# Performance work log

Hardware: AMD Instinct MI355X
Metric: run time of the kernel (lower is better)

The kernel has to match this reference:

```python
import jax, jax.numpy as jnp
import numpy as np

EMA_DECAY = 0.99
LOSS_SCALE = 10.0
COMMIT_COEF = 0.25
EPS = 1e-5


def setup_inputs() -> dict:
    key = jax.random.key(0)
    k1, k2, k3 = jax.random.split(key, 3)
    B, S, D, K = 8, 2048, 256, 4096
    z = jax.random.normal(k1, (B, S, D), dtype=jnp.float32)
    attention_mask = jnp.ones((B, S), dtype=jnp.float32)
    codebook = jax.random.normal(k2, (K, D), dtype=jnp.float32)
    ema_count = jnp.ones((K,), dtype=jnp.float32)
    ema_weight = codebook.copy()  # torch: ema_weight = codebook.weight.data.clone()
    return {"z": z, "attention_mask": attention_mask, "codebook": codebook,
            "ema_count": ema_count, "ema_weight": ema_weight}


def reference(z, attention_mask, codebook, ema_count, ema_weight):
    B, S, D = z.shape
    K = codebook.shape[0]
    flat = z.reshape(-1, D)                       # [N, D], N = B*S
    # squared euclidean distances to codebook: [N, K]
    distances = (jnp.sum(flat * flat, axis=1, keepdims=True)
                 - 2.0 * flat @ codebook.T
                 + jnp.sum(codebook * codebook, axis=1))
    indices = jnp.argmin(distances, axis=1)       # [N] int
    quantized = codebook[indices].reshape(B, S, D)

    # EMA accumulation (training path). Instead of materializing the NxK
    # one-hot and doing encodings.T @ flat, use segment sums (same math).
    mask_flat = attention_mask.reshape(-1)        # [N]
    n = jax.ops.segment_sum(mask_flat, indices, num_segments=K)            # [K]
    dw = jax.ops.segment_sum(flat * mask_flat[:, None], indices,
                             num_segments=K)                               # [K, D]

    new_count = ema_count * EMA_DECAY + (1.0 - EMA_DECAY) * n
    total = jnp.sum(new_count)
    new_count = (new_count + EPS) / (total + K * EPS) * total
    new_weight = ema_weight * EMA_DECAY + (1.0 - EMA_DECAY) * dw

    # commitment loss (quantized detached)
    loss_tok = jnp.mean((z - jax.lax.stop_gradient(quantized)) ** 2, axis=-1)  # [B,S]
    quantize_loss = LOSS_SCALE * COMMIT_COEF * jnp.sum(loss_tok * attention_mask) / jnp.sum(attention_mask)

    # straight-through estimator
    out = z + jax.lax.stop_gradient(quantized - z)
    return out, indices, quantize_loss, new_count, new_weight
```

## Files before the change

### kernel.cpp

```cpp
#include <hip/hip_runtime.h>
#include <hip/hip_fp16.h>
#include <cstdint>
#include <cstddef>


#define N_TOK 16384
#define DIM   256
#define K_CB  4096

typedef _Float16 h8    __attribute__((ext_vector_type(8)));
typedef float    f32x4 __attribute__((ext_vector_type(4)));
typedef float    f32x16 __attribute__((ext_vector_type(16)));

#define WS_ZF      0u
#define WS_CP      8388608u
#define WS_CN      10485760u
#define WS_NRM     10502144u
#define WS_CAND    10630144u
#define WS_IDX     12727296u
#define WS_COUNT   12792832u
#define WS_START   12809216u
#define WS_CURSOR  12825616u
#define WS_SORTED  12842000u
#define WS_NACC    16921600u
#define WS_NB      16937984u
#define WS_LPART   16938000u
#define WS_MPART   16954384u
#define WS_NBPART  16970768u

__device__ __forceinline__ void gload_lds16(const void* g, void* l) {
  __builtin_amdgcn_global_load_lds(
      (const __attribute__((address_space(1))) uint32_t*)g,
      (__attribute__((address_space(3))) uint32_t*)l, 16, 0, 0);
}

__global__ void vq_split_z(const float* __restrict__ z, unsigned short* __restrict__ zf,
                           float2* __restrict__ nrm) {
  int t = blockIdx.x * 256 + threadIdx.x;
  int tok = t >> 5, c = t & 31;
  const float4* zp = reinterpret_cast<const float4*>(z) + (size_t)tok * 64 + c * 2;
  float4 va = zp[0], vb = zp[1];
  float x[8] = {va.x, va.y, va.z, va.w, vb.x, vb.y, vb.z, vb.w};
  union { _Float16 h[8]; uint4 u; } a;
  float s1 = 0.f, s2 = 0.f;
#pragma unroll
  for (int i = 0; i < 8; ++i) {
    _Float16 h1 = (_Float16)x[i];
    float lo = (x[i] - (float)h1) * 2048.0f;
    a.h[i] = h1;
    s1 += (float)h1 * (float)h1;
    s2 += lo * lo;
  }
  size_t off = (size_t)(tok >> 7) * 65536u + (size_t)(c >> 1) * 4096u
             + (size_t)(tok & 127) * 32u + (size_t)(c & 1) * 16u;
  *reinterpret_cast<uint4*>((unsigned char*)zf + off) = a.u;
#pragma unroll
  for (int o = 1; o < 32; o <<= 1) { s1 += __shfl_xor(s1, o); s2 += __shfl_xor(s2, o); }
  if (c == 0) nrm[tok] = make_float2(sqrtf(s1), sqrtf(s2));
}

__global__ void vq_split_c(const float* __restrict__ cb, unsigned short* __restrict__ cp1,
                           float* __restrict__ cn1, float2* __restrict__ nbpart) {
  __shared__ float sm1[4], sm2[4];
  int w = threadIdx.x >> 6, l = threadIdx.x & 63;
  int row = blockIdx.x * 4 + w;
  float4 v = reinterpret_cast<const float4*>(cb)[row * 64 + l];
  float x[4] = {v.x, v.y, v.z, v.w};
  union { _Float16 h[4]; ushort4 u; } a;
  double ss = 0.0;
  float s1 = 0.f, s2 = 0.f;
#pragma unroll
  for (int i = 0; i < 4; ++i) {
    _Float16 h1 = (_Float16)x[i];
    float lo = (x[i] - (float)h1) * 2048.0f;
    a.h[i] = h1;
    s1 += (float)h1 * (float)h1;
    s2 += lo * lo;
    ss += (double)x[i] * (double)x[i];
  }
  reinterpret_cast<ushort4*>(cp1)[row * 64 + l] = a.u;
  for (int off = 1; off < 64; off <<= 1) {
    s1 += __shfl_xor(s1, off); s2 += __shfl_xor(s2, off); ss += __shfl_xor(ss, off);
  }
  if (l == 0) {
    cn1[row] = (float)ss;
    sm1[w] = s1; sm2[w] = s2;
  }
  __syncthreads();
  if (threadIdx.x == 0) {
    float m1 = fmaxf(fmaxf(sm1[0], sm1[1]), fmaxf(sm1[2], sm1[3]));
    float m2 = fmaxf(fmaxf(sm2[0], sm2[1]), fmaxf(sm2[2], sm2[3]));
    nbpart[blockIdx.x] = make_float2(sqrtf(m1), sqrtf(m2));
  }
}

__global__ void vq_nb_reduce(const float2* __restrict__ nbpart, float* __restrict__ nb) {
  __shared__ float r1[256], r2[256];
  int tid = threadIdx.x;
  float m1 = 0.f, m2 = 0.f;
  for (int i = tid; i < 1024; i += 256) {
    float2 p = nbpart[i];
    m1 = fmaxf(m1, p.x); m2 = fmaxf(m2, p.y);
  }
  r1[tid] = m1; r2[tid] = m2; __syncthreads();
  for (int s = 128; s > 0; s >>= 1) {
    if (tid < s) { r1[tid] = fmaxf(r1[tid], r1[tid + s]); r2[tid] = fmaxf(r2[tid], r2[tid + s]); }
    __syncthreads();
  }
  if (tid == 0) { nb[0] = r1[0]; nb[1] = r2[0]; }
}

__global__ __launch_bounds__(256, 2) void vq_scan(
    const unsigned short* __restrict__ zf, const unsigned short* __restrict__ cp,
    const float* __restrict__ cn1, float4* __restrict__ cand) {
  __shared__ __align__(1024) unsigned char cbl[2][16384];
  __shared__ __align__(16) float cnl[2][32];

  const int bid  = blockIdx.x;
  const int wgid = (bid & 7) * 128 + (bid >> 3);
  const int tg   = wgid >> 3;
  const int es   = wgid & 7;
  const int tok0 = tg * 128;
  const int e0b  = es * 512;

  const int tx = threadIdx.x;
  const int w = tx >> 6, l = tx & 63;
  const int r = l & 31, h = l >> 5;

  const unsigned char* zg = (const unsigned char*)zf + (size_t)tg * 65536u
                            + (unsigned)(w * 1024 + r * 32 + h * 16);
  h8 zfr[16];
#pragma unroll
  for (int kt = 0; kt < 16; ++kt) {
    const void* p = zg + kt * 4096;
    asm volatile("global_load_dwordx4 %0, %1, off"
                 : "=v"(zfr[kt]) : "v"(p));
  }

  const unsigned char* cpb = (const unsigned char*)cp;

  float v1 = 3e38f, v2 = 3e38f;
  int   i1 = 0x7fffffff, i2 = 0x7fffffff;

#pragma unroll
  for (int j = 0; j < 4; ++j) {
    int row = (w * 4 + j) * 2 + h;
    int lc  = r ^ row;
    gload_lds16(cpb + (size_t)(e0b + row) * 512 + lc * 16,
                &cbl[0][(w * 4 + j) * 1024]);
  }
  if (tx < 8)
    gload_lds16((const unsigned char*)cn1 + (size_t)e0b * 4 + tx * 16, &cnl[0][0]);
  __syncthreads();

  for (int t = 0; t < 16; ++t) {
    const int b = t & 1;
    if (t < 15) {
      const int e0n = e0b + (t + 1) * 32;
#pragma unroll
      for (int j = 0; j < 4; ++j) {
        int row = (w * 4 + j) * 2 + h;
        int lc  = r ^ row;
        gload_lds16(cpb + (size_t)(e0n + row) * 512 + lc * 16,
                    &cbl[b ^ 1][(w * 4 + j) * 1024]);
      }
      if (tx < 8)
        gload_lds16((const unsigned char*)cn1 + (size_t)e0n * 4 + tx * 16,
                    &cnl[b ^ 1][0]);
    }

    f32x16 acc;
#pragma unroll
    for (int i = 0; i < 16; ++i) acc[i] = 0.f;
#pragma unroll
    for (int kt = 0; kt < 16; ++kt) {
      int sc = (kt * 2 + h) ^ r;
      h8 af = *reinterpret_cast<const h8*>(&cbl[b][r * 512 + sc * 16]);
      acc = __builtin_amdgcn_mfma_f32_32x32x16_f16(af, zfr[kt], acc, 0, 0, 0);
    }

    const int e0 = e0b + t * 32 + 4 * h;
#pragma unroll
    for (int g = 0; g < 4; ++g) {
      f32x4 cnv = *reinterpret_cast<const f32x4*>(&cnl[b][g * 8 + 4 * h]);
#pragma unroll
      for (int q = 0; q < 4; ++q) {
        float d = cnv[q] - 2.0f * acc[g * 4 + q];
        int   e = e0 + g * 8 + q;
        bool c1 = d < v1, c2 = d < v2;
        i2 = c1 ? i1 : (c2 ? e : i2);
        v2 = c1 ? v1 : (c2 ? d : v2);
        i1 = c1 ? e : i1;
        v1 = c1 ? d : v1;
      }
    }
    __syncthreads();
  }

  {
    float ov1 = __shfl_xor(v1, 32), ov2 = __shfl_xor(v2, 32);
    int   oi1 = __shfl_xor(i1, 32), oi2 = __shfl_xor(i2, 32);
    if (ov1 < v1 || (ov1 == v1 && oi1 < i1)) {
      v2 = v1; i2 = i1; v1 = ov1; i1 = oi1;
    } else if (ov1 < v2 || (ov1 == v2 && oi1 < i2)) {
      v2 = ov1; i2 = oi1;
    }
    if (ov2 < v1 || (ov2 == v1 && oi2 < i1)) {
      v2 = v1; i2 = i1; v1 = ov2; i1 = oi2;
    } else if (ov2 < v2 || (ov2 == v2 && oi2 < i2)) {
      v2 = ov2; i2 = oi2;
    }
    if (h == 0) {
      int token = tok0 + w * 32 + r;
      cand[(size_t)token * 8 + es] =
          make_float4(v1, v2, __int_as_float(i1), __int_as_float(i2));
    }
  }
}

__global__ void vq_merge(
    const float4* __restrict__ cand, const float* __restrict__ z,
    const float* __restrict__ mask, const float* __restrict__ codebook,
    const float2* __restrict__ nrm, const float* __restrict__ nb,
    float* __restrict__ out0, float* __restrict__ out_idx,
    int* __restrict__ idxs, int* __restrict__ count,
    float* __restrict__ loss_part, float* __restrict__ mask_part) {
  __shared__ float ls[4], ms[4];
  int w = threadIdx.x >> 6, l = threadIdx.x & 63;
  int token = blockIdx.x * 4 + w;

  float4 rec = cand[(size_t)token * 8 + (l & 7)];
  float rv1 = rec.x, rv2 = rec.y;
  int   ri1 = __float_as_int(rec.z), ri2 = __float_as_int(rec.w);
  float m_a = rv1;
  for (int o = 1; o < 8; o <<= 1) m_a = fminf(m_a, __shfl_xor(m_a, o));

  float2 nh = nrm[token];
  float NB1 = nb[0], NB2 = nb[1];
  float E = 2.0f * ((nh.x * NB2 + nh.y * NB1) * (1.0f / 2048.0f)
                    + nh.y * NB2 * (1.0f / 4194304.0f));
  float thr = m_a + 2.0f * E * 1.05f + 0.05f;

  float4 zv = reinterpret_cast<const float4*>(z)[(size_t)token * 64 + l];

  unsigned long long c1 = __ballot((l < 8) && (rv1 <= thr));
  unsigned long long c2 = __ballot((l < 8) && (rv2 <= thr));
  double bd = 1e300; int bi = 0x7fffffff;
  while (c1 | c2) {
    int k;
    if (c1) { int s = __ffsll(c1) - 1; c1 &= c1 - 1; k = __shfl(ri1, s); }
    else    { int s = __ffsll(c2) - 1; c2 &= c2 - 1; k = __shfl(ri2, s); }
    float4 cv = reinterpret_cast<const float4*>(codebook)[(size_t)k * 64 + l];
    double d0 = (double)zv.x - cv.x, d1 = (double)zv.y - cv.y;
    double d2 = (double)zv.z - cv.z, d3 = (double)zv.w - cv.w;
    double dd = d0 * d0 + d1 * d1 + d2 * d2 + d3 * d3;
    for (int o = 1; o < 64; o <<= 1) dd += __shfl_xor(dd, o);
    if (dd < bd || (dd == bd && k < bi)) { bd = dd; bi = k; }
  }

  float4 cv = reinterpret_cast<const float4*>(codebook)[(size_t)bi * 64 + l];
  reinterpret_cast<float4*>(out0)[(size_t)token * 64 + l] = cv;

  float mk = mask[token];
  if (l == 0) {
    out_idx[token] = (float)bi;
    idxs[token]    = bi;
    atomicAdd(&count[bi], 1);
    ls[w] = mk * (float)bd * (1.0f / 256.0f);
    ms[w] = mk;
  }
  __syncthreads();
  if (threadIdx.x == 0) {
    loss_part[blockIdx.x] = ls[0] + ls[1] + ls[2] + ls[3];
    mask_part[blockIdx.x] = ms[0] + ms[1] + ms[2] + ms[3];
  }
}

__global__ void vq_prescan(const int* __restrict__ count, int* __restrict__ start,
                           int* __restrict__ cursor) {
  __shared__ int wsum[256];
  int tid = threadIdx.x;
  int loc[16]; int s = 0;
#pragma unroll
  for (int i = 0; i < 16; ++i) { loc[i] = count[tid * 16 + i]; s += loc[i]; }
  wsum[tid] = s;
  __syncthreads();
  for (int off = 1; off < 256; off <<= 1) {
    int v = (tid >= off) ? wsum[tid - off] : 0;
    __syncthreads();
    wsum[tid] += v;
    __syncthreads();
  }
  int run = wsum[tid] - s;
#pragma unroll
  for (int i = 0; i < 16; ++i) {
    start[tid * 16 + i]  = run;
    cursor[tid * 16 + i] = run;
    run += loc[i];
  }
  if (tid == 255) start[K_CB] = wsum[255];
}

__global__ void vq_scatter(const int* __restrict__ idxs, int* __restrict__ cursor,
                           int* __restrict__ sorted) {
  int t = blockIdx.x * 256 + threadIdx.x;
  int k = idxs[t];
  int pos = atomicAdd(&cursor[k], 1);
  sorted[pos] = t;
}

__global__ __launch_bounds__(512) void vq_segsum(
    const int* __restrict__ start, const int* __restrict__ sorted,
    const float* __restrict__ z, const float* __restrict__ mask,
    const float* __restrict__ ew,
    float* __restrict__ out_weight, float* __restrict__ nacc) {
  __shared__ float4 red[8][64];
  __shared__ float nas[8];
  const int k = blockIdx.x;
  const int w = threadIdx.x >> 6, l = threadIdx.x & 63;
  const int s = start[k], e = start[k + 1];
  const float4* z4 = reinterpret_cast<const float4*>(z);

  float ax = 0.f, ay = 0.f, az = 0.f, aw = 0.f, na = 0.f;
  int i = s + w;
  for (; i + 8 < e; i += 16) {
    int t0 = sorted[i], t1 = sorted[i + 8];
    float mk0 = mask[t0], mk1 = mask[t1];
    float4 a4 = z4[(size_t)t0 * 64 + l];
    float4 b4 = z4[(size_t)t1 * 64 + l];
    ax += mk0 * a4.x + mk1 * b4.x;
    ay += mk0 * a4.y + mk1 * b4.y;
    az += mk0 * a4.z + mk1 * b4.z;
    aw += mk0 * a4.w + mk1 * b4.w;
    na += mk0 + mk1;
  }
  if (i < e) {
    int t0 = sorted[i];
    float mk0 = mask[t0];
    float4 a4 = z4[(size_t)t0 * 64 + l];
    ax += mk0 * a4.x; ay += mk0 * a4.y; az += mk0 * a4.z; aw += mk0 * a4.w;
    na += mk0;
  }
  red[w][l] = make_float4(ax, ay, az, aw);
  if (l == 0) nas[w] = na;
  __syncthreads();

  if (w == 0) {
    float4 a = red[0][l];
#pragma unroll
    for (int j = 1; j < 8; ++j) {
      float4 b = red[j][l];
      a.x += b.x; a.y += b.y; a.z += b.z; a.w += b.w;
    }
    float4 e4 = reinterpret_cast<const float4*>(ew)[(size_t)k * 64 + l];
    float4 o;
    o.x = 0.99f * e4.x + 0.01f * a.x;
    o.y = 0.99f * e4.y + 0.01f * a.y;
    o.z = 0.99f * e4.z + 0.01f * a.z;
    o.w = 0.99f * e4.w + 0.01f * a.w;
    reinterpret_cast<float4*>(out_weight)[(size_t)k * 64 + l] = o;
    if (l == 0) {
      float nn = 0.f;
#pragma unroll
      for (int j = 0; j < 8; ++j) nn += nas[j];
      nacc[k] = nn;
    }
  }
}

__global__ void vq_finish_count(const float* __restrict__ ec, const float* __restrict__ nacc,
                                const float* __restrict__ loss_part,
                                const float* __restrict__ mask_part,
                                float* __restrict__ out_count, float* __restrict__ out_loss) {
  __shared__ float nc_s[K_CB];
  __shared__ float red[256];
  int tid = threadIdx.x;
  float part = 0.f;
  for (int i = tid; i < K_CB; i += 256) {
    float nc = 0.99f * ec[i] + 0.01f * nacc[i];
    nc_s[i] = nc; part += nc;
  }
  red[tid] = part; __syncthreads();
  for (int s = 128; s > 0; s >>= 1) { if (tid < s) red[tid] += red[tid + s]; __syncthreads(); }
  float total = red[0];
  float scale = total / (total + (float)K_CB * 1e-5f);
  for (int i = tid; i < K_CB; i += 256) out_count[i] = (nc_s[i] + 1e-5f) * scale;
  __syncthreads();

  float ln = 0.f, lm = 0.f;
  for (int i = tid; i < 4096; i += 256) { ln += loss_part[i]; lm += mask_part[i]; }
  red[tid] = ln; __syncthreads();
  for (int s = 128; s > 0; s >>= 1) { if (tid < s) red[tid] += red[tid + s]; __syncthreads(); }
  ln = red[0]; __syncthreads();
  red[tid] = lm; __syncthreads();
  for (int s = 128; s > 0; s >>= 1) { if (tid < s) red[tid] += red[tid + s]; __syncthreads(); }
  lm = red[0];
  if (tid == 0) out_loss[0] = 2.5f * ln / lm;
}

extern "C" void kernel_launch(void* const* d_in, const int* in_sizes, int n_in,
                              void* d_out, int out_size, void* d_ws, size_t ws_size,
                              hipStream_t stream) {
  const float* z          = (const float*)d_in[0];
  const float* mask       = (const float*)d_in[1];
  const float* codebook   = (const float*)d_in[2];
  const float* ema_count  = (const float*)d_in[3];
  const float* ema_weight = (const float*)d_in[4];

  float* out        = (float*)d_out;
  float* out0       = out;
  float* out_idx    = out + 4194304;
  float* out_loss   = out + 4210688;
  float* out_count  = out + 4210689;
  float* out_weight = out + 4214785;

  char* ws = (char*)d_ws;
  unsigned short* zf  = (unsigned short*)(ws + WS_ZF);
  unsigned short* cp1 = (unsigned short*)(ws + WS_CP);
  float*  cn1    = (float*) (ws + WS_CN);
  float2* nrm    = (float2*)(ws + WS_NRM);
  float4* cand   = (float4*)(ws + WS_CAND);
  int*    idxs   = (int*)   (ws + WS_IDX);
  int*    count  = (int*)   (ws + WS_COUNT);
  int*    startp = (int*)   (ws + WS_START);
  int*    cursor = (int*)   (ws + WS_CURSOR);
  int*    sorted = (int*)   (ws + WS_SORTED);
  float*  nacc   = (float*) (ws + WS_NACC);
  float*  nbmax  = (float*) (ws + WS_NB);
  float*  lpart  = (float*) (ws + WS_LPART);
  float*  mpart  = (float*) (ws + WS_MPART);
  float2* nbpart = (float2*)(ws + WS_NBPART);

  (void)hipMemsetAsync(ws + WS_COUNT, 0, 16384, stream);

  vq_split_z<<<2048, 256, 0, stream>>>(z, zf, nrm);
  vq_split_c<<<1024, 256, 0, stream>>>(codebook, cp1, cn1, nbpart);
  vq_nb_reduce<<<1, 256, 0, stream>>>(nbpart, nbmax);
  vq_scan<<<1024, 256, 0, stream>>>(zf, cp1, cn1, cand);
  vq_merge<<<4096, 256, 0, stream>>>(cand, z, mask, codebook, nrm, nbmax,
                                     out0, out_idx, idxs, count, lpart, mpart);
  vq_prescan<<<1, 256, 0, stream>>>(count, startp, cursor);
  vq_scatter<<<64, 256, 0, stream>>>(idxs, cursor, sorted);
  vq_segsum<<<4096, 512, 0, stream>>>(startp, sorted, z, mask, ema_weight,
                                      out_weight, nacc);
  vq_finish_count<<<1, 256, 0, stream>>>(ema_count, nacc, lpart, mpart,
                                         out_count, out_loss);
}
```

Before: 127.1 us.

## Pack top-2 candidates into sortable keys and overlap selection with next MFMA tile

```diff
diff --git a/kernel.cpp b/kernel.cpp
--- a/kernel.cpp
+++ b/kernel.cpp
@@ -112,7 +112,8 @@
 
 __global__ __launch_bounds__(256, 2) void vq_scan(
     const unsigned short* __restrict__ zf, const unsigned short* __restrict__ cp,
-    const float* __restrict__ cn1, float4* __restrict__ cand) {
+    const float* __restrict__ cn1, const float2* __restrict__ nrm,
+    float2* __restrict__ cand) {
   __shared__ __align__(1024) unsigned char cbl[2][16384];
   __shared__ __align__(16) float cnl[2][32];
 
@@ -136,90 +137,101 @@
     asm volatile("global_load_dwordx4 %0, %1, off"
                  : "=v"(zfr[kt]) : "v"(p));
   }
+  float znr = nrm[tok0 + w * 32 + r].x;
+  const float zn = znr * znr;
 
   const unsigned char* cpb = (const unsigned char*)cp;
-
-  float v1 = 3e38f, v2 = 3e38f;
-  int   i1 = 0x7fffffff, i2 = 0x7fffffff;
-
-#pragma unroll
-  for (int j = 0; j < 4; ++j) {
-    int row = (w * 4 + j) * 2 + h;
-    int lc  = r ^ row;
-    gload_lds16(cpb + (size_t)(e0b + row) * 512 + lc * 16,
-                &cbl[0][(w * 4 + j) * 1024]);
-  }
-  if (tx < 8)
-    gload_lds16((const unsigned char*)cn1 + (size_t)e0b * 4 + tx * 16, &cnl[0][0]);
-  __syncthreads();
-
-  for (int t = 0; t < 16; ++t) {
-    const int b = t & 1;
-    if (t < 15) {
-      const int e0n = e0b + (t + 1) * 32;
-#pragma unroll
-      for (int j = 0; j < 4; ++j) {
-        int row = (w * 4 + j) * 2 + h;
-        int lc  = r ^ row;
-        gload_lds16(cpb + (size_t)(e0n + row) * 512 + lc * 16,
-                    &cbl[b ^ 1][(w * 4 + j) * 1024]);
-      }
-      if (tx < 8)
-        gload_lds16((const unsigned char*)cn1 + (size_t)e0n * 4 + tx * 16,
-                    &cnl[b ^ 1][0]);
-    }
-
-    f32x16 acc;
-#pragma unroll
-    for (int i = 0; i < 16; ++i) acc[i] = 0.f;
-#pragma unroll
-    for (int kt = 0; kt < 16; ++kt) {
-      int sc = (kt * 2 + h) ^ r;
-      h8 af = *reinterpret_cast<const h8*>(&cbl[b][r * 512 + sc * 16]);
-      acc = __builtin_amdgcn_mfma_f32_32x32x16_f16(af, zfr[kt], acc, 0, 0, 0);
-    }
-
-    const int e0 = e0b + t * 32 + 4 * h;
-#pragma unroll
-    for (int g = 0; g < 4; ++g) {
-      f32x4 cnv = *reinterpret_cast<const f32x4*>(&cnl[b][g * 8 + 4 * h]);
-#pragma unroll
-      for (int q = 0; q < 4; ++q) {
-        float d = cnv[q] - 2.0f * acc[g * 4 + q];
-        int   e = e0 + g * 8 + q;
-        bool c1 = d < v1, c2 = d < v2;
-        i2 = c1 ? i1 : (c2 ? e : i2);
-        v2 = c1 ? v1 : (c2 ? d : v2);
-        i1 = c1 ? e : i1;
-        v1 = c1 ? d : v1;
-      }
-    }
-    __syncthreads();
-  }
+  unsigned lo = 0xFFFFFFFFu, hi = 0xFFFFFFFFu;
+
+#define STAGE(T1)                                                           \
+  {                                                                         \
+    const int e0n = e0b + (T1) * 32;                                        \
+    _Pragma("unroll")                                                       \
+    for (int j = 0; j < 4; ++j) {                                           \
+      int row = (w * 4 + j) * 2 + h;                                        \
+      int lc  = r ^ row;                                                    \
+      gload_lds16(cpb + (size_t)(e0n + row) * 512 + lc * 16,                \
+                  &cbl[(T1) & 1][(w * 4 + j) * 1024]);                      \
+    }                                                                       \
+    if (tx < 8)                                                             \
+      gload_lds16((const unsigned char*)cn1 + (size_t)e0n * 4 + tx * 16,    \
+                  &cnl[(T1) & 1][0]);                                       \
+  }
+
+#define INIT_ACC(C, BUF)                                                    \
+  {                                                                         \
+    _Pragma("unroll")                                                       \
+    for (int g = 0; g < 4; ++g) {                                           \
+      f32x4 cnv = *reinterpret_cast<const f32x4*>(&cnl[(BUF)][g * 8 + 4 * h]); \
+      _Pragma("unroll")                                                     \
+      for (int q = 0; q < 4; ++q) (C)[g * 4 + q] = -0.5f * (zn + cnv[q]);   \
+    }                                                                       \
+  }
+
+#define MFMA_TILE(C, BUF)                                                   \
+  {                                                                         \
+    _Pragma("unroll")                                                       \
+    for (int kt = 0; kt < 16; ++kt) {                                       \
+      int sc = (kt * 2 + h) ^ r;                                            \
+      h8 af = *reinterpret_cast<const h8*>(&cbl[(BUF)][r * 512 + sc * 16]); \
+      (C) = __builtin_amdgcn_mfma_f32_32x32x16_f16(af, zfr[kt], (C), 0, 0, 0); \
+    }                                                                       \
+  }
+
+#define SELECT_PREV(P, TPREV)                                               \
+  {                                                                         \
+    _Pragma("unroll")                                                       \
+    for (int i = 0; i < 16; ++i) {                                          \
+      float d = -2.0f * (P)[i];                                             \
+      unsigned eloc = (unsigned)((TPREV) * 32 + ((i & 3) + 8 * (i >> 2) + 4 * h)); \
+      unsigned key = (__float_as_uint(d) & 0xFFFFFE00u) | eloc;             \
+      unsigned mx = lo > key ? lo : key;                                    \
+      lo = lo < key ? lo : key;                                             \
+      hi = hi < mx ? hi : mx;                                               \
+    }                                                                       \
+  }
+
+#define TILE_BODY(T, CUR, PRV, DOSEL)                                       \
+  {                                                                         \
+    if ((T) < 15) STAGE((T) + 1);                                           \
+    INIT_ACC(CUR, (T) & 1);                                                 \
+    MFMA_TILE(CUR, (T) & 1);                                                \
+    if (DOSEL) SELECT_PREV(PRV, (T) - 1);                                   \
+    __syncthreads();                                                        \
+  }
+
+  STAGE(0);
+  __syncthreads();
+
+  f32x16 accA, accB;
+  for (int tt = 0; tt < 8; ++tt) {
+    TILE_BODY(2 * tt,     accA, accB, (tt > 0));
+    TILE_BODY(2 * tt + 1, accB, accA, true);
+  }
+  SELECT_PREV(accB, 15);
+
+#undef TILE_BODY
+#undef SELECT_PREV
+#undef MFMA_TILE
+#undef INIT_ACC
+#undef STAGE
 
   {
-    float ov1 = __shfl_xor(v1, 32), ov2 = __shfl_xor(v2, 32);
-    int   oi1 = __shfl_xor(i1, 32), oi2 = __shfl_xor(i2, 32);
-    if (ov1 < v1 || (ov1 == v1 && oi1 < i1)) {
-      v2 = v1; i2 = i1; v1 = ov1; i1 = oi1;
-    } else if (ov1 < v2 || (ov1 == v2 && oi1 < i2)) {
-      v2 = ov1; i2 = oi1;
-    }
-    if (ov2 < v1 || (ov2 == v1 && oi2 < i1)) {
-      v2 = v1; i2 = i1; v1 = ov2; i1 = oi2;
-    } else if (ov2 < v2 || (ov2 == v2 && oi2 < i2)) {
-      v2 = ov2; i2 = oi2;
-    }
+    unsigned olo = __shfl_xor(lo, 32), ohi = __shfl_xor(hi, 32);
+    unsigned mx = lo > olo ? lo : olo;
+    lo = lo < olo ? lo : olo;
+    hi = hi < ohi ? hi : ohi;
+    hi = hi < mx ? hi : mx;
     if (h == 0) {
       int token = tok0 + w * 32 + r;
       cand[(size_t)token * 8 + es] =
-          make_float4(v1, v2, __int_as_float(i1), __int_as_float(i2));
+          make_float2(__uint_as_float(lo), __uint_as_float(hi));
     }
   }
 }
 
 __global__ void vq_merge(
-    const float4* __restrict__ cand, const float* __restrict__ z,
+    const float2* __restrict__ cand, const float* __restrict__ z,
     const float* __restrict__ mask, const float* __restrict__ codebook,
     const float2* __restrict__ nrm, const float* __restrict__ nb,
     float* __restrict__ out0, float* __restrict__ out_idx,
@@ -229,9 +241,12 @@
   int w = threadIdx.x >> 6, l = threadIdx.x & 63;
   int token = blockIdx.x * 4 + w;
 
-  float4 rec = cand[(size_t)token * 8 + (l & 7)];
-  float rv1 = rec.x, rv2 = rec.y;
-  int   ri1 = __float_as_int(rec.z), ri2 = __float_as_int(rec.w);
+  float2 rec = cand[(size_t)token * 8 + (l & 7)];
+  unsigned k1 = __float_as_uint(rec.x), k2 = __float_as_uint(rec.y);
+  float rv1 = __uint_as_float(k1 & 0xFFFFFE00u);
+  float rv2 = __uint_as_float(k2 & 0xFFFFFE00u);
+  int   ri1 = (l & 7) * 512 + (int)(k1 & 0x1FFu);
+  int   ri2 = (l & 7) * 512 + (int)(k2 & 0x1FFu);
   float m_a = rv1;
   for (int o = 1; o < 8; o <<= 1) m_a = fminf(m_a, __shfl_xor(m_a, o));
 
@@ -239,7 +254,7 @@
   float NB1 = nb[0], NB2 = nb[1];
   float E = 2.0f * ((nh.x * NB2 + nh.y * NB1) * (1.0f / 2048.0f)
                     + nh.y * NB2 * (1.0f / 4194304.0f));
-  float thr = m_a + 2.0f * E * 1.05f + 0.05f;
+  float thr = m_a * 1.0001f + 2.0f * E * 1.05f + 0.1f;
 
   float4 zv = reinterpret_cast<const float4*>(z)[(size_t)token * 64 + l];
 
@@ -419,7 +434,7 @@
   unsigned short* cp1 = (unsigned short*)(ws + WS_CP);
   float*  cn1    = (float*) (ws + WS_CN);
   float2* nrm    = (float2*)(ws + WS_NRM);
-  float4* cand   = (float4*)(ws + WS_CAND);
+  float2* cand   = (float2*)(ws + WS_CAND);
   int*    idxs   = (int*)   (ws + WS_IDX);
   int*    count  = (int*)   (ws + WS_COUNT);
   int*    startp = (int*)   (ws + WS_START);
@@ -436,7 +451,7 @@
   vq_split_z<<<2048, 256, 0, stream>>>(z, zf, nrm);
   vq_split_c<<<1024, 256, 0, stream>>>(codebook, cp1, cn1, nbpart);
   vq_nb_reduce<<<1, 256, 0, stream>>>(nbpart, nbmax);
-  vq_scan<<<1024, 256, 0, stream>>>(zf, cp1, cn1, cand);
+  vq_scan<<<1024, 256, 0, stream>>>(zf, cp1, cn1, nrm, cand);
   vq_merge<<<4096, 256, 0, stream>>>(cand, z, mask, codebook, nrm, nbmax,
                                      out0, out_idx, idxs, count, lpart, mpart);
   vq_prescan<<<1, 256, 0, stream>>>(count, startp, cursor);
```

Result: no change. 125.1 us (-1.6%).
